# Kernel optimization log

Measured on AMD Instinct MI355X. Metric: run time of the kernel, lower is better.

The kernel has to match this reference:

```python
import jax, jax.numpy as jnp
import numpy as np


def _extract_patches(x, k):
    # x: [H, W, C] -> [H, W, k*k, C], SAME zero padding, stride 1 (tf.image.extract_patches semantics)
    H, W, C = x.shape
    p0 = (k - 1) // 2
    p1 = k - 1 - p0
    xp = jnp.pad(x, ((p0, p1), (p0, p1), (0, 0)))
    # fixed k*k shifts (k is a static Python int), vectorized over H, W, C
    return jnp.stack([xp[i:i + H, j:j + W] for i in range(k) for j in range(k)], axis=2)


def setup_inputs() -> dict:
    key = jax.random.key(0)
    k1, k2, k3 = jax.random.split(key, 3)
    H, W, C = 256, 256, 32
    return {
        "main": jax.random.normal(k1, (H, W, C), dtype=jnp.float32),
        "ref": jax.random.normal(k2, (H, W, C), dtype=jnp.float32),
        "ref_value": jax.random.normal(k3, (H, W, C), dtype=jnp.float32),
        "k_size": 7,
    }


def reference(main, ref, ref_value, k_size):
    # windowed local attention ('dot' mode):
    # score[h,w,p] = <ref_patch[h,w,p,:], main[h,w,:]>, softmax over p (k*k window),
    # out[h,w,c]   = sum_p attn[h,w,p] * ref_value_patch[h,w,p,c]
    ref_patches = _extract_patches(ref, k_size)        # [H, W, k^2, C]
    val_patches = _extract_patches(ref_value, k_size)  # [H, W, k^2, C]
    scores = jnp.einsum("hwpc,hwc->hwp", ref_patches, main)
    attn = jax.nn.softmax(scores, axis=-1)             # softmax over the k^2 window
    return jnp.einsum("hwp,hwpc->hwc", attn, val_patches)  # [H, W, C]
```

## Files before the change

kernel.cpp:

```cpp
#include <hip/hip_runtime.h>

#define HH 256
#define WW 256
#define CC 32
#define K 7
#define RAD 3
#define TS 16
#define HALO (TS + K - 1)
#define NP (HALO * HALO)
#define PIX_STRIDE 40

typedef _Float16 h2 __attribute__((ext_vector_type(2)));
typedef float f2 __attribute__((ext_vector_type(2)));
typedef float f4 __attribute__((ext_vector_type(4)));
typedef unsigned int u32;
typedef u32 u2v __attribute__((ext_vector_type(2)));
typedef u32 u4v __attribute__((ext_vector_type(4)));

union U4H {
    u4v u;
    h2 h[4];
};

static __device__ inline h2 pkrtz(float x, float y) {
    auto t = __builtin_amdgcn_cvt_pkrtz(x, y);
    h2 r;
    __builtin_memcpy(&r, &t, sizeof(r));
    return r;
}

static __device__ inline u32 pkrtz_u(float x, float y) {
    auto t = __builtin_amdgcn_cvt_pkrtz(x, y);
    u32 r;
    __builtin_memcpy(&r, &t, sizeof(r));
    return r;
}

static __device__ inline float fdot2f(h2 a, h2 b, float c) {
#if __has_builtin(__builtin_amdgcn_fdot2)
    return __builtin_amdgcn_fdot2(a, b, c, false);
#else
    return c + (float)a[0] * (float)b[0] + (float)a[1] * (float)b[1];
#endif
}

__global__ __launch_bounds__(256) void local_attn_kernel(
    const float* __restrict__ main_in,
    const float* __restrict__ ref_in,
    const float* __restrict__ val_in,
    float* __restrict__ out)
{
    __shared__ ushort s_ref[NP * PIX_STRIDE];
    __shared__ ushort s_val[NP * PIX_STRIDE];

    const int tid = threadIdx.x;
    const int ox = blockIdx.x * TS;
    const int oy = blockIdx.y * TS;

    for (int idx = tid; idx < NP * 8; idx += 256) {
        const int pix = idx >> 3;
        const int c4 = idx & 7;
        const int hh = pix / HALO;
        const int ww = pix - hh * HALO;
        const int gh = oy + hh - RAD;
        const int gw = ox + ww - RAD;
        u2v r_out = {0u, 0u};
        u2v v_out = {0u, 0u};
        if ((unsigned)gh < (unsigned)HH && (unsigned)gw < (unsigned)WW) {
            const long goff = ((long)(gh * WW + gw)) * CC + c4 * 4;
            f4 r = *(const f4*)(ref_in + goff);
            f4 v = *(const f4*)(val_in + goff);
            r_out[0] = pkrtz_u(r.x, r.y);
            r_out[1] = pkrtz_u(r.z, r.w);
            v_out[0] = pkrtz_u(v.x, v.y);
            v_out[1] = pkrtz_u(v.z, v.w);
        }
        *(u2v*)(&s_ref[pix * PIX_STRIDE + c4 * 4]) = r_out;
        *(u2v*)(&s_val[pix * PIX_STRIDE + c4 * 4]) = v_out;
    }

    __syncthreads();

    const int tx = tid & 15;
    const int ty = tid >> 4;
    const int gh = oy + ty;
    const int gw = ox + tx;

    const f4* mp = (const f4*)(main_in + ((long)(gh * WW + gw)) * CC);
    h2 mh[16];
#pragma unroll
    for (int q = 0; q < 8; ++q) {
        f4 m = mp[q];
        mh[2 * q]     = pkrtz(m.x, m.y);
        mh[2 * q + 1] = pkrtz(m.z, m.w);
    }

    float s[K * K];
#pragma unroll
    for (int di = 0; di < K; ++di) {
#pragma unroll
        for (int dj = 0; dj < K; ++dj) {
            const ushort* base = &s_ref[((ty + di) * HALO + (tx + dj)) * PIX_STRIDE];
            float acc = 0.0f;
#pragma unroll
            for (int u = 0; u < 4; ++u) {
                U4H q;
                q.u = *(const u4v*)(base + u * 8);
                acc = fdot2f(q.h[0], mh[4 * u + 0], acc);
                acc = fdot2f(q.h[1], mh[4 * u + 1], acc);
                acc = fdot2f(q.h[2], mh[4 * u + 2], acc);
                acc = fdot2f(q.h[3], mh[4 * u + 3], acc);
            }
            s[di * K + dj] = acc;
        }
    }

    float m = s[0];
#pragma unroll
    for (int p = 1; p < K * K; ++p) m = fmaxf(m, s[p]);
    float l = 0.0f;
#pragma unroll
    for (int p = 0; p < K * K; ++p) {
        s[p] = __expf(s[p] - m);
        l += s[p];
    }

    h2 acc[16];
#pragma unroll
    for (int j = 0; j < 16; ++j) acc[j] = h2{(_Float16)0, (_Float16)0};

#pragma unroll
    for (int di = 0; di < K; ++di) {
#pragma unroll
        for (int dj = 0; dj < K; ++dj) {
            const float wf = s[di * K + dj];
            const h2 wh = pkrtz(wf, wf);
            const ushort* base = &s_val[((ty + di) * HALO + (tx + dj)) * PIX_STRIDE];
#pragma unroll
            for (int u = 0; u < 4; ++u) {
                U4H q;
                q.u = *(const u4v*)(base + u * 8);
                acc[4 * u + 0] += wh * q.h[0];
                acc[4 * u + 1] += wh * q.h[1];
                acc[4 * u + 2] += wh * q.h[2];
                acc[4 * u + 3] += wh * q.h[3];
            }
        }
    }

    const float invl = 1.0f / l;
    float* op = out + ((long)(gh * WW + gw)) * CC;
#pragma unroll
    for (int j = 0; j < 16; ++j) {
        f2 o;
        o.x = (float)acc[j][0] * invl;
        o.y = (float)acc[j][1] * invl;
        *(f2*)(op + 2 * j) = o;
    }
}

extern "C" void kernel_launch(void* const* d_in, const int* in_sizes, int n_in,
                              void* d_out, int out_size, void* d_ws, size_t ws_size,
                              hipStream_t stream) {
    const float* main_in = (const float*)d_in[0];
    const float* ref_in  = (const float*)d_in[1];
    const float* val_in  = (const float*)d_in[2];
    float* o = (float*)d_out;
    dim3 grid(WW / TS, HH / TS);
    local_attn_kernel<<<grid, dim3(256), 0, stream>>>(main_in, ref_in, val_in, o);
}
```

Measured before the change: 89.63 us.

## Split each pixel's 49-tap window across four lanes with shuffle reductions

Each output pixel is now handled by four threads, and each thread takes every fourth window position (13 taps instead of 49). The row-max and sum for the softmax are combined with xor shuffles, and the fp16 channel accumulators are reduced with a butterfly exchange so each lane writes 8 channels. The tile becomes 16x8 pixels with 512 threads, which shrinks the halo tile in LDS but raises the redundant halo fraction. The goal is to cut per-thread register pressure and serial work and to raise parallelism, at the cost of shuffle overhead, more halo reloads and main-vector loads repeated across the four lanes.

```diff
diff --git a/kernel.cpp b/kernel.cpp
--- a/kernel.cpp
+++ b/kernel.cpp
@@ -5,13 +5,15 @@
 #define CC 32
 #define K 7
 #define RAD 3
-#define TS 16
-#define HALO (TS + K - 1)
-#define NP (HALO * HALO)
+#define TSX 16
+#define TSY 8
+#define HX (TSX + K - 1)
+#define HY (TSY + K - 1)
+#define NP (HX * HY)
 #define PIX_STRIDE 40
+#define NTHREADS 512
 
 typedef _Float16 h2 __attribute__((ext_vector_type(2)));
-typedef float f2 __attribute__((ext_vector_type(2)));
 typedef float f4 __attribute__((ext_vector_type(4)));
 typedef unsigned int u32;
 typedef u32 u2v __attribute__((ext_vector_type(2)));
@@ -44,7 +46,16 @@
 #endif
 }
 
-__global__ __launch_bounds__(256) void local_attn_kernel(
+static __device__ inline h2 shfl_xor_h2(h2 v, int mask) {
+    int b;
+    __builtin_memcpy(&b, &v, 4);
+    b = __shfl_xor(b, mask);
+    h2 r;
+    __builtin_memcpy(&r, &b, 4);
+    return r;
+}
+
+__global__ __launch_bounds__(NTHREADS) void local_attn_kernel(
     const float* __restrict__ main_in,
     const float* __restrict__ ref_in,
     const float* __restrict__ val_in,
@@ -54,16 +65,16 @@
     __shared__ ushort s_val[NP * PIX_STRIDE];
 
     const int tid = threadIdx.x;
-    const int ox = blockIdx.x * TS;
-    const int oy = blockIdx.y * TS;
-
-    for (int idx = tid; idx < NP * 8; idx += 256) {
+    const int ox = blockIdx.x * TSX;
+    const int oy = blockIdx.y * TSY;
+
+    for (int idx = tid; idx < NP * 8; idx += NTHREADS) {
         const int pix = idx >> 3;
         const int c4 = idx & 7;
-        const int hh = pix / HALO;
-        const int ww = pix - hh * HALO;
-        const int gh = oy + hh - RAD;
-        const int gw = ox + ww - RAD;
+        const int hy = pix / HX;
+        const int wx = pix - hy * HX;
+        const int gh = oy + hy - RAD;
+        const int gw = ox + wx - RAD;
         u2v r_out = {0u, 0u};
         u2v v_out = {0u, 0u};
         if ((unsigned)gh < (unsigned)HH && (unsigned)gw < (unsigned)WW) {
@@ -81,10 +92,11 @@
 
     __syncthreads();
 
-    const int tx = tid & 15;
-    const int ty = tid >> 4;
-    const int gh = oy + ty;
-    const int gw = ox + tx;
+    const int sub = tid & 3;
+    const int px = (tid >> 2) & 15;
+    const int py = tid >> 6;
+    const int gh = oy + py;
+    const int gw = ox + px;
 
     const f4* mp = (const f4*)(main_in + ((long)(gh * WW + gw)) * CC);
     h2 mh[16];
@@ -95,12 +107,15 @@
         mh[2 * q + 1] = pkrtz(m.z, m.w);
     }
 
-    float s[K * K];
-#pragma unroll
-    for (int di = 0; di < K; ++di) {
-#pragma unroll
-        for (int dj = 0; dj < K; ++dj) {
-            const ushort* base = &s_ref[((ty + di) * HALO + (tx + dj)) * PIX_STRIDE];
+    float w[13];
+    float mymax = -1e30f;
+#pragma unroll
+    for (int t = 0; t < 13; ++t) {
+        const int p = 4 * t + sub;
+        if (4 * t + 3 < 49 || p < 49) {
+            const int di = p / 7;
+            const int dj = p - di * 7;
+            const ushort* base = &s_ref[((py + di) * HX + (px + dj)) * PIX_STRIDE];
             float acc = 0.0f;
 #pragma unroll
             for (int u = 0; u < 4; ++u) {
@@ -111,31 +126,41 @@
                 acc = fdot2f(q.h[2], mh[4 * u + 2], acc);
                 acc = fdot2f(q.h[3], mh[4 * u + 3], acc);
             }
-            s[di * K + dj] = acc;
-        }
-    }
-
-    float m = s[0];
-#pragma unroll
-    for (int p = 1; p < K * K; ++p) m = fmaxf(m, s[p]);
-    float l = 0.0f;
-#pragma unroll
-    for (int p = 0; p < K * K; ++p) {
-        s[p] = __expf(s[p] - m);
-        l += s[p];
-    }
+            w[t] = acc;
+            mymax = fmaxf(mymax, acc);
+        }
+    }
+
+    float m = mymax;
+    m = fmaxf(m, __shfl_xor(m, 1));
+    m = fmaxf(m, __shfl_xor(m, 2));
+
+    float lp = 0.0f;
+#pragma unroll
+    for (int t = 0; t < 13; ++t) {
+        const int p = 4 * t + sub;
+        if (4 * t + 3 < 49 || p < 49) {
+            w[t] = __expf(w[t] - m);
+            lp += w[t];
+        }
+    }
+    float l = lp;
+    l += __shfl_xor(l, 1);
+    l += __shfl_xor(l, 2);
 
     h2 acc[16];
 #pragma unroll
     for (int j = 0; j < 16; ++j) acc[j] = h2{(_Float16)0, (_Float16)0};
 
 #pragma unroll
-    for (int di = 0; di < K; ++di) {
-#pragma unroll
-        for (int dj = 0; dj < K; ++dj) {
-            const float wf = s[di * K + dj];
+    for (int t = 0; t < 13; ++t) {
+        const int p = 4 * t + sub;
+        if (4 * t + 3 < 49 || p < 49) {
+            const int di = p / 7;
+            const int dj = p - di * 7;
+            const float wf = w[t];
             const h2 wh = pkrtz(wf, wf);
-            const ushort* base = &s_val[((ty + di) * HALO + (tx + dj)) * PIX_STRIDE];
+            const ushort* base = &s_val[((py + di) * HX + (px + dj)) * PIX_STRIDE];
 #pragma unroll
             for (int u = 0; u < 4; ++u) {
                 U4H q;
@@ -148,15 +173,35 @@
         }
     }
 
+    const bool hi1 = (sub & 1) != 0;
+#pragma unroll
+    for (int j = 0; j < 8; ++j) {
+        h2 mine   = hi1 ? acc[j + 8] : acc[j];
+        h2 theirs = shfl_xor_h2(hi1 ? acc[j] : acc[j + 8], 1);
+        acc[j] = mine + theirs;
+    }
+    const bool hi2 = (sub & 2) != 0;
+#pragma unroll
+    for (int j = 0; j < 4; ++j) {
+        h2 mine   = hi2 ? acc[j + 4] : acc[j];
+        h2 theirs = shfl_xor_h2(hi2 ? acc[j] : acc[j + 4], 2);
+        acc[j] = mine + theirs;
+    }
+    const int chan_base = ((sub & 1) << 4) + ((sub & 2) << 2);
+
     const float invl = 1.0f / l;
-    float* op = out + ((long)(gh * WW + gw)) * CC;
-#pragma unroll
-    for (int j = 0; j < 16; ++j) {
-        f2 o;
-        o.x = (float)acc[j][0] * invl;
-        o.y = (float)acc[j][1] * invl;
-        *(f2*)(op + 2 * j) = o;
-    }
+    float* op = out + ((long)(gh * WW + gw)) * CC + chan_base;
+    f4 o0, o1;
+    o0.x = (float)acc[0][0] * invl;
+    o0.y = (float)acc[0][1] * invl;
+    o0.z = (float)acc[1][0] * invl;
+    o0.w = (float)acc[1][1] * invl;
+    o1.x = (float)acc[2][0] * invl;
+    o1.y = (float)acc[2][1] * invl;
+    o1.z = (float)acc[3][0] * invl;
+    o1.w = (float)acc[3][1] * invl;
+    *(f4*)(op)     = o0;
+    *(f4*)(op + 4) = o1;
 }
 
 extern "C" void kernel_launch(void* const* d_in, const int* in_sizes, int n_in,
@@ -166,6 +211,6 @@
     const float* ref_in  = (const float*)d_in[1];
     const float* val_in  = (const float*)d_in[2];
     float* o = (float*)d_out;
-    dim3 grid(WW / TS, HH / TS);
-    local_attn_kernel<<<grid, dim3(256), 0, stream>>>(main_in, ref_in, val_in, o);
-}
+    dim3 grid(WW / TSX, HH / TSY);
+    local_attn_kernel<<<grid, dim3(NTHREADS), 0, stream>>>(main_in, ref_in, val_in, o);
+}
```

New measurement: 84.08 us. 6.2% less time.

## Compute windowed attention with MFMA banded matmuls over row strips

Applied to the files above, without the earlier changes.

Replaces the per-thread fdot2 score loop and half2 value accumulation with 16x16x32 f16 MFMA instructions. Each wavefront handles a row of 16 pixels, computes banded score tiles per window row and masks out-of-window entries. The value tile is stored transposed in shared memory so the probability-times-value product can also run on MFMA. Tiles change to 16x8 with zero-initialised LDS. This trades the scalar ALU dot products for matrix-core work, at the cost of wasted MFMA lanes on masked entries, transposed scalar LDS stores and an extra zeroing pass.

```diff
diff --git a/kernel.cpp b/kernel.cpp
--- a/kernel.cpp
+++ b/kernel.cpp
@@ -5,157 +5,158 @@
 #define CC 32
 #define K 7
 #define RAD 3
-#define TS 16
-#define HALO (TS + K - 1)
-#define NP (HALO * HALO)
-#define PIX_STRIDE 40
+#define TSX 16
+#define TSY 8
+#define HX (TSX + K - 1)
+#define HY (TSY + K - 1)
+#define NPIX (HX * HY)
+#define REF_ST 40
+#define REF_SZ 12800
+#define VT_ST 344
+#define VT_SZ 11008
+#define NTHREADS 256
 
-typedef _Float16 h2 __attribute__((ext_vector_type(2)));
-typedef float f2 __attribute__((ext_vector_type(2)));
+typedef _Float16 half_t;
+typedef _Float16 h8 __attribute__((ext_vector_type(8)));
 typedef float f4 __attribute__((ext_vector_type(4)));
 typedef unsigned int u32;
+typedef u32 u4v __attribute__((ext_vector_type(4)));
 typedef u32 u2v __attribute__((ext_vector_type(2)));
-typedef u32 u4v __attribute__((ext_vector_type(4)));
 
-union U4H {
-    u4v u;
-    h2 h[4];
-};
-
-static __device__ inline h2 pkrtz(float x, float y) {
-    auto t = __builtin_amdgcn_cvt_pkrtz(x, y);
-    h2 r;
-    __builtin_memcpy(&r, &t, sizeof(r));
-    return r;
-}
+union Frag { h8 h; u4v u; u32 w[4]; };
 
 static __device__ inline u32 pkrtz_u(float x, float y) {
     auto t = __builtin_amdgcn_cvt_pkrtz(x, y);
-    u32 r;
-    __builtin_memcpy(&r, &t, sizeof(r));
-    return r;
+    u32 r; __builtin_memcpy(&r, &t, sizeof(r)); return r;
 }
 
-static __device__ inline float fdot2f(h2 a, h2 b, float c) {
-#if __has_builtin(__builtin_amdgcn_fdot2)
-    return __builtin_amdgcn_fdot2(a, b, c, false);
-#else
-    return c + (float)a[0] * (float)b[0] + (float)a[1] * (float)b[1];
-#endif
-}
-
-__global__ __launch_bounds__(256) void local_attn_kernel(
+__global__ __launch_bounds__(NTHREADS) void local_attn_mfma(
     const float* __restrict__ main_in,
     const float* __restrict__ ref_in,
     const float* __restrict__ val_in,
     float* __restrict__ out)
 {
-    __shared__ ushort s_ref[NP * PIX_STRIDE];
-    __shared__ ushort s_val[NP * PIX_STRIDE];
+    __shared__ half_t s_ref[REF_SZ];
+    __shared__ half_t s_valT[VT_SZ];
 
     const int tid = threadIdx.x;
-    const int ox = blockIdx.x * TS;
-    const int oy = blockIdx.y * TS;
+    const int ox = blockIdx.x * TSX;
+    const int oy = blockIdx.y * TSY;
 
-    for (int idx = tid; idx < NP * 8; idx += 256) {
+    for (int j = tid; j < REF_SZ / 2; j += NTHREADS) ((u32*)s_ref)[j] = 0u;
+    for (int j = tid; j < VT_SZ / 2; j += NTHREADS) ((u32*)s_valT)[j] = 0u;
+    __syncthreads();
+
+    for (int idx = tid; idx < NPIX * 8; idx += NTHREADS) {
         const int pix = idx >> 3;
         const int c4 = idx & 7;
-        const int hh = pix / HALO;
-        const int ww = pix - hh * HALO;
-        const int gh = oy + hh - RAD;
-        const int gw = ox + ww - RAD;
-        u2v r_out = {0u, 0u};
-        u2v v_out = {0u, 0u};
+        const int hy = pix / HX;
+        const int wx = pix - hy * HX;
+        const int gh = oy + hy - RAD;
+        const int gw = ox + wx - RAD;
+        u32 r0 = 0, r1 = 0;
+        f4 v = {0.f, 0.f, 0.f, 0.f};
         if ((unsigned)gh < (unsigned)HH && (unsigned)gw < (unsigned)WW) {
-            const long goff = ((long)(gh * WW + gw)) * CC + c4 * 4;
-            f4 r = *(const f4*)(ref_in + goff);
-            f4 v = *(const f4*)(val_in + goff);
-            r_out[0] = pkrtz_u(r.x, r.y);
-            r_out[1] = pkrtz_u(r.z, r.w);
-            v_out[0] = pkrtz_u(v.x, v.y);
-            v_out[1] = pkrtz_u(v.z, v.w);
+            const int goff = (gh * WW + gw) * CC + c4 * 4;
+            f4 rv = *(const f4*)(ref_in + goff);
+            v = *(const f4*)(val_in + goff);
+            r0 = pkrtz_u(rv.x, rv.y);
+            r1 = pkrtz_u(rv.z, rv.w);
         }
-        *(u2v*)(&s_ref[pix * PIX_STRIDE + c4 * 4]) = r_out;
-        *(u2v*)(&s_val[pix * PIX_STRIDE + c4 * 4]) = v_out;
+        u2v rw = {r0, r1};
+        *(u2v*)(s_ref + pix * REF_ST + c4 * 4) = rw;
+        const int ch = c4 * 4;
+        const int vo = hy * 24 + wx;
+        s_valT[(ch + 0) * VT_ST + vo] = (half_t)v.x;
+        s_valT[(ch + 1) * VT_ST + vo] = (half_t)v.y;
+        s_valT[(ch + 2) * VT_ST + vo] = (half_t)v.z;
+        s_valT[(ch + 3) * VT_ST + vo] = (half_t)v.w;
     }
-
     __syncthreads();
 
-    const int tx = tid & 15;
-    const int ty = tid >> 4;
-    const int gh = oy + ty;
-    const int gw = ox + tx;
+    const int lane = tid & 63;
+    const int i = lane & 15;
+    const int g = lane >> 4;
+    const int k0 = 8 * (i >> 2) + (i & 3);
+    const int d0 = 8 * g - i;
+    const int wv = tid >> 6;
 
-    const f4* mp = (const f4*)(main_in + ((long)(gh * WW + gw)) * CC);
-    h2 mh[16];
+#pragma unroll 1
+    for (int rrow = 0; rrow < 2; ++rrow) {
+        const int hl = 2 * wv + rrow;
+        const int h = oy + hl;
+
+        const float* qp = main_in + (h * WW + ox + i) * CC + g * 8;
+        f4 q0 = *(const f4*)qp;
+        f4 q1 = *(const f4*)(qp + 4);
+        Frag qf;
+        qf.w[0] = pkrtz_u(q0.x, q0.y);
+        qf.w[1] = pkrtz_u(q0.z, q0.w);
+        qf.w[2] = pkrtz_u(q1.x, q1.y);
+        qf.w[3] = pkrtz_u(q1.z, q1.w);
+
+        float sc[K][8];
 #pragma unroll
-    for (int q = 0; q < 8; ++q) {
-        f4 m = mp[q];
-        mh[2 * q]     = pkrtz(m.x, m.y);
-        mh[2 * q + 1] = pkrtz(m.z, m.w);
-    }
-
-    float s[K * K];
+        for (int di = 0; di < K; ++di) {
+            const int rb = (hl + di) * HX;
+            const int p0 = rb + k0;
+            const int p1 = p0 + 4;
+            Frag a0, a1;
+            a0.u = *(const u4v*)(s_ref + p0 * REF_ST + g * 8);
+            a1.u = *(const u4v*)(s_ref + p1 * REF_ST + g * 8);
+            f4 c1a = {0.f, 0.f, 0.f, 0.f};
+            f4 c1b = {0.f, 0.f, 0.f, 0.f};
+            c1a = __builtin_amdgcn_mfma_f32_16x16x32_f16(a0.h, qf.h, c1a, 0, 0, 0);
+            c1b = __builtin_amdgcn_mfma_f32_16x16x32_f16(a1.h, qf.h, c1b, 0, 0, 0);
 #pragma unroll
-    for (int di = 0; di < K; ++di) {
-#pragma unroll
-        for (int dj = 0; dj < K; ++dj) {
-            const ushort* base = &s_ref[((ty + di) * HALO + (tx + dj)) * PIX_STRIDE];
-            float acc = 0.0f;
-#pragma unroll
-            for (int u = 0; u < 4; ++u) {
-                U4H q;
-                q.u = *(const u4v*)(base + u * 8);
-                acc = fdot2f(q.h[0], mh[4 * u + 0], acc);
-                acc = fdot2f(q.h[1], mh[4 * u + 1], acc);
-                acc = fdot2f(q.h[2], mh[4 * u + 2], acc);
-                acc = fdot2f(q.h[3], mh[4 * u + 3], acc);
-            }
-            s[di * K + dj] = acc;
-        }
-    }
-
-    float m = s[0];
-#pragma unroll
-    for (int p = 1; p < K * K; ++p) m = fmaxf(m, s[p]);
-    float l = 0.0f;
-#pragma unroll
-    for (int p = 0; p < K * K; ++p) {
-        s[p] = __expf(s[p] - m);
-        l += s[p];
-    }
-
-    h2 acc[16];
-#pragma unroll
-    for (int j = 0; j < 16; ++j) acc[j] = h2{(_Float16)0, (_Float16)0};
-
-#pragma unroll
-    for (int di = 0; di < K; ++di) {
-#pragma unroll
-        for (int dj = 0; dj < K; ++dj) {
-            const float wf = s[di * K + dj];
-            const h2 wh = pkrtz(wf, wf);
-            const ushort* base = &s_val[((ty + di) * HALO + (tx + dj)) * PIX_STRIDE];
-#pragma unroll
-            for (int u = 0; u < 4; ++u) {
-                U4H q;
-                q.u = *(const u4v*)(base + u * 8);
-                acc[4 * u + 0] += wh * q.h[0];
-                acc[4 * u + 1] += wh * q.h[1];
-                acc[4 * u + 2] += wh * q.h[2];
-                acc[4 * u + 3] += wh * q.h[3];
+            for (int r = 0; r < 4; ++r) {
+                sc[di][r]     = ((unsigned)(d0 + r) <= 6u)     ? c1a[r] : -1e30f;
+                sc[di][r + 4] = ((unsigned)(d0 + 4 + r) <= 6u) ? c1b[r] : -1e30f;
             }
         }
-    }
 
-    const float invl = 1.0f / l;
-    float* op = out + ((long)(gh * WW + gw)) * CC;
+        float mx = -1e30f;
 #pragma unroll
-    for (int j = 0; j < 16; ++j) {
-        f2 o;
-        o.x = (float)acc[j][0] * invl;
-        o.y = (float)acc[j][1] * invl;
-        *(f2*)(op + 2 * j) = o;
+        for (int di = 0; di < K; ++di)
+#pragma unroll
+            for (int j = 0; j < 8; ++j) mx = fmaxf(mx, sc[di][j]);
+        mx = fmaxf(mx, __shfl_xor(mx, 16));
+        mx = fmaxf(mx, __shfl_xor(mx, 32));
+        float lsum = 0.f;
+#pragma unroll
+        for (int di = 0; di < K; ++di)
+#pragma unroll
+            for (int j = 0; j < 8; ++j) {
+                const float ev = __expf(sc[di][j] - mx);
+                sc[di][j] = ev;
+                lsum += ev;
+            }
+        lsum += __shfl_xor(lsum, 16);
+        lsum += __shfl_xor(lsum, 32);
+        const float invl = 1.0f / lsum;
+
+        f4 c2a = {0.f, 0.f, 0.f, 0.f};
+        f4 c2b = {0.f, 0.f, 0.f, 0.f};
+#pragma unroll
+        for (int di = 0; di < K; ++di) {
+            Frag pf;
+            pf.w[0] = pkrtz_u(sc[di][0], sc[di][1]);
+            pf.w[1] = pkrtz_u(sc[di][2], sc[di][3]);
+            pf.w[2] = pkrtz_u(sc[di][4], sc[di][5]);
+            pf.w[3] = pkrtz_u(sc[di][6], sc[di][7]);
+            const int ro = (hl + di) * 24 + g * 8;
+            Frag va0, va1;
+            va0.u = *(const u4v*)(s_valT + i * VT_ST + ro);
+            va1.u = *(const u4v*)(s_valT + (i + 16) * VT_ST + ro);
+            c2a = __builtin_amdgcn_mfma_f32_16x16x32_f16(va0.h, pf.h, c2a, 0, 0, 0);
+            c2b = __builtin_amdgcn_mfma_f32_16x16x32_f16(va1.h, pf.h, c2b, 0, 0, 0);
+        }
+
+        float* op = out + (h * WW + ox + i) * CC;
+        f4 o0 = {c2a[0] * invl, c2a[1] * invl, c2a[2] * invl, c2a[3] * invl};
+        f4 o1 = {c2b[0] * invl, c2b[1] * invl, c2b[2] * invl, c2b[3] * invl};
+        *(f4*)(op + 4 * g) = o0;
+        *(f4*)(op + 16 + 4 * g) = o1;
     }
 }
 
@@ -166,6 +167,6 @@
     const float* ref_in  = (const float*)d_in[1];
     const float* val_in  = (const float*)d_in[2];
     float* o = (float*)d_out;
-    dim3 grid(WW / TS, HH / TS);
-    local_attn_kernel<<<grid, dim3(256), 0, stream>>>(main_in, ref_in, val_in, o);
+    dim3 grid(WW / TSX, HH / TSY);
+    local_attn_mfma<<<grid, dim3(NTHREADS), 0, stream>>>(main_in, ref_in, val_in, o);
 }
```

Measured after the change: 84.88 us. -5.3%, faster.
